# Kernel optimization log

Measured on AMD Instinct MI355X. Metric: run time of the kernel, lower is better.

## Reference

```python
import jax, jax.numpy as jnp
import numpy as np
import math

B, T, D = 2, 2048, 1024
DC, DM, H = 512, 1536, 16
DE, DG = 4096, 1024
EPS = 1e-5
NEG = -1e30


def _layernorm(x, w, b):
    mu = jnp.mean(x, axis=-1, keepdims=True)
    var = jnp.mean(jnp.square(x - mu), axis=-1, keepdims=True)
    return (x - mu) * jax.lax.rsqrt(var + EPS) * w + b


def setup_inputs() -> dict:
    key = jax.random.key(0)
    ks = jax.random.split(key, 12)
    s = 0.02
    x = jax.random.normal(ks[0], (B, T, D), jnp.float32)
    mask = jnp.tril(jnp.ones((T, T), jnp.int32))[None, None]  # [1,1,T,T] causal
    return {
        "x": x,
        "mask": mask,
        "ln1_w": jnp.ones((D,), jnp.float32),
        "ln1_b": jnp.zeros((D,), jnp.float32),
        "wq": jax.random.normal(ks[1], (D, DC), jnp.float32) * s,
        "bq": jnp.zeros((DC,), jnp.float32),
        "wk": jax.random.normal(ks[2], (D, DC), jnp.float32) * s,
        "bk": jnp.zeros((DC,), jnp.float32),
        "wv": jax.random.normal(ks[3], (D, DM), jnp.float32) * s,
        "bv": jnp.zeros((DM,), jnp.float32),
        "wo": jax.random.normal(ks[4], (DM, D), jnp.float32) * s,
        "bo": jnp.zeros((D,), jnp.float32),
        "ln2_w": jnp.ones((D,), jnp.float32),
        "ln2_b": jnp.zeros((D,), jnp.float32),
        "we": jax.random.normal(ks[5], (D, DE), jnp.float32) * s,
        "be": jnp.zeros((DE,), jnp.float32),
        "wg": jax.random.normal(ks[6], (D, DG), jnp.float32) * s,
        "bg": jnp.zeros((DG,), jnp.float32),
        "wu": jax.random.normal(ks[7], (DG, DE), jnp.float32) * s,
        "bu": jnp.zeros((DE,), jnp.float32),
        "wc": jax.random.normal(ks[8], (DE, D), jnp.float32) * s,
        "bc": jnp.zeros((D,), jnp.float32),
    }


def reference(x, mask, ln1_w, ln1_b, wq, bq, wk, bk, wv, bv, wo, bo,
              ln2_w, ln2_b, we, be, wg, bg, wu, bu, wc, bc):
    b, t, _ = x.shape
    chd, mhd = DC // H, DM // H
    # --- attention sublayer ---
    x1 = _layernorm(x, ln1_w, ln1_b)
    q = (x1 @ wq + bq).reshape(b, t, H, chd).transpose(0, 2, 1, 3)  # [b,h,t,chd]
    k = (x1 @ wk + bk).reshape(b, t, H, chd).transpose(0, 2, 1, 3)
    v = (x1 @ wv + bv).reshape(b, t, H, mhd).transpose(0, 2, 1, 3)  # [b,h,t,mhd]
    sc = jnp.einsum('bhqd,bhkd->bhqk', q, k) / math.sqrt(chd)
    sc = jnp.where(mask == 0, NEG, sc)
    attn = jax.nn.softmax(sc, axis=-1)
    y = jnp.einsum('bhqk,bhkd->bhqd', attn, v)  # [b,h,t,mhd]
    y = y.transpose(0, 2, 1, 3).reshape(b, t, DM)
    x = x + (y @ wo + bo)
    # --- FFN sublayer (double-gated SiLU) ---
    x2 = _layernorm(x, ln2_w, ln2_b)
    e = x2 @ we + be
    g = jax.nn.sigmoid(jax.nn.silu(x2 @ wg + bg) @ wu + bu)
    return x + (jax.nn.silu(e * g) @ wc + bc)
```

## Files before the change

### kernel.cpp

```cpp
#include <hip/hip_runtime.h>
#include <hip/hip_bf16.h>

typedef __bf16 bf16x8_t __attribute__((ext_vector_type(8)));
typedef float f32x4_t __attribute__((ext_vector_type(4)));

#define B_ 2
#define T_ 2048
#define D_ 1024
#define DC_ 512
#define DM_ 1536
#define H_ 16
#define DE_ 4096
#define DG_ 1024
#define ROWS (B_*T_)
#define QS_ 2560
#define EG_ 5120
#define MB (1u<<20)

#define GPTR(p) ((const __attribute__((address_space(1))) unsigned int*)(p))
#define LPTR(p) ((__attribute__((address_space(3))) unsigned int*)(p))

__device__ __forceinline__ float sigmoid_f(float x) { return 1.f / (1.f + __expf(-x)); }

__global__ __launch_bounds__(256)
void transpose_cast(const float* __restrict__ W, __hip_bfloat16* __restrict__ Wt,
                    int K, int N) {
    __shared__ float t[32][33];
    const int n0 = blockIdx.x * 32, k0 = blockIdx.y * 32;
    const int tx = threadIdx.x, ty = threadIdx.y;
#pragma unroll
    for (int r = 0; r < 4; ++r)
        t[ty + r * 8][tx] = W[(size_t)(k0 + ty + r * 8) * N + n0 + tx];
    __syncthreads();
#pragma unroll
    for (int r = 0; r < 4; ++r)
        Wt[(size_t)(n0 + ty + r * 8) * K + k0 + tx] = __float2bfloat16(t[tx][ty + r * 8]);
}

__global__ __launch_bounds__(256)
void concat_bias3(const float* __restrict__ a, int na, const float* __restrict__ b,
                  int nb, const float* __restrict__ c, int n, float* __restrict__ o) {
    const int i = blockIdx.x * 256 + threadIdx.x;
    if (i < n)
        o[i] = i < na ? a[i] : (i < na + nb ? b[i - na] : c[i - na - nb]);
}

__global__ __launch_bounds__(256)
void transpose_v(const __hip_bfloat16* __restrict__ QKV, __hip_bfloat16* __restrict__ Vt) {
    __shared__ __hip_bfloat16 t[32][33];
    const int bh = blockIdx.z;
    const int b = bh >> 4, h = bh & 15;
    const int t0 = blockIdx.x * 32;
    const int d0 = blockIdx.y * 32;
    const int tx = threadIdx.x, ty = threadIdx.y;
#pragma unroll
    for (int r = 0; r < 4; ++r)
        t[ty + r * 8][tx] = QKV[(size_t)(b * T_ + t0 + ty + r * 8) * QS_ + 1024 + h * 96 + d0 + tx];
    __syncthreads();
#pragma unroll
    for (int r = 0; r < 4; ++r)
        Vt[((size_t)bh * 96 + d0 + ty + r * 8) * T_ + t0 + tx] = t[tx][ty + r * 8];
}

__global__ __launch_bounds__(256)
void ln_cast(const float* __restrict__ x, const float* __restrict__ w,
             const float* __restrict__ b, __hip_bfloat16* __restrict__ out) {
    const int row = blockIdx.x;
    const int tid = threadIdx.x;
    const float4 v = ((const float4*)(x + (size_t)row * D_))[tid];
    float s = v.x + v.y + v.z + v.w;
#pragma unroll
    for (int o = 32; o; o >>= 1) s += __shfl_down(s, o);
    __shared__ float red1[4], red2[4];
    if (!(tid & 63)) red1[tid >> 6] = s;
    __syncthreads();
    const float mu = (red1[0] + red1[1] + red1[2] + red1[3]) * (1.f / D_);
    const float dx = v.x - mu, dy = v.y - mu, dz = v.z - mu, dw = v.w - mu;
    float s2 = dx * dx + dy * dy + dz * dz + dw * dw;
#pragma unroll
    for (int o = 32; o; o >>= 1) s2 += __shfl_down(s2, o);
    if (!(tid & 63)) red2[tid >> 6] = s2;
    __syncthreads();
    const float var = (red2[0] + red2[1] + red2[2] + red2[3]) * (1.f / D_);
    const float rs = rsqrtf(var + 1e-5f);
    const float4 wv = ((const float4*)w)[tid];
    const float4 bv = ((const float4*)b)[tid];
    __hip_bfloat16* op = out + (size_t)row * D_ + tid * 4;
    op[0] = __float2bfloat16(dx * rs * wv.x + bv.x);
    op[1] = __float2bfloat16(dy * rs * wv.y + bv.y);
    op[2] = __float2bfloat16(dz * rs * wv.z + bv.z);
    op[3] = __float2bfloat16(dw * rs * wv.w + bv.w);
}

template <int EPI, int BM, int BN>
__global__ __launch_bounds__(256)
void gemm_bt(const __hip_bfloat16* __restrict__ A, const __hip_bfloat16* __restrict__ Bt,
             const float* __restrict__ bias, const float* __restrict__ resid,
             const __hip_bfloat16* __restrict__ Ein,
             void* __restrict__ C0, void* __restrict__ C1, int M, int N, int K) {
    constexpr int MI = BM / 32, NJ = BN / 32;
    constexpr size_t STAGE_BYTES = (size_t)(BM + BN) * 128;
    constexpr size_t EPI_BYTES = (EPI == 1) ? (size_t)BM * (BN + 4) * 4
                                            : (size_t)BM * (BN + 8) * 2;
    constexpr size_t SMEM_BYTES = STAGE_BYTES > EPI_BYTES ? STAGE_BYTES : EPI_BYTES;
    __shared__ __align__(16) unsigned char smem[SMEM_BYTES];
    __hip_bfloat16* As0 = (__hip_bfloat16*)smem;
    __hip_bfloat16* Bs0 = As0 + BM * 32;
    __hip_bfloat16* As1 = Bs0 + BN * 32;
    __hip_bfloat16* Bs1 = As1 + BM * 32;

    const int tid = threadIdx.x;
    const int m0 = blockIdx.y * BM;
    const int n0 = blockIdx.x * BN;
    const int lane = tid & 63;
    const int wave = tid >> 6;
    const int wm = (wave >> 1) * (BM / 2), wn = (wave & 1) * (BN / 2);
    const int quad = lane >> 4;
    const int lr = lane & 15;

    auto stage = [&](int k0, __hip_bfloat16* Asd, __hip_bfloat16* Bsd) {
#pragma unroll
        for (int p = 0; p < BM / 64; ++p) {
            const int s = p * 256 + tid;
            const int row = s >> 2;
            const int kc2 = (s & 3) ^ ((row >> 1) & 3);
            __builtin_amdgcn_global_load_lds(
                GPTR(A + (size_t)(m0 + row) * K + k0 + kc2 * 8),
                LPTR(Asd + s * 8), 16, 0, 0);
        }
#pragma unroll
        for (int p = 0; p < BN / 64; ++p) {
            const int s = p * 256 + tid;
            const int row = s >> 2;
            const int kc2 = (s & 3) ^ ((row >> 1) & 3);
            __builtin_amdgcn_global_load_lds(
                GPTR(Bt + (size_t)(n0 + row) * K + k0 + kc2 * 8),
                LPTR(Bsd + s * 8), 16, 0, 0);
        }
    };

    f32x4_t acc[MI][NJ] = {};
    stage(0, As0, Bs0);
    const int kiters = K >> 5;
    for (int k = 0; k < kiters; ++k) {
        __syncthreads();
        const __hip_bfloat16* Ar = (k & 1) ? As1 : As0;
        const __hip_bfloat16* Br = (k & 1) ? Bs1 : Bs0;
        if (k + 1 < kiters)
            stage((k + 1) << 5, (k & 1) ? As0 : As1, (k & 1) ? Bs0 : Bs1);
        bf16x8_t af[MI], bfr[NJ];
#pragma unroll
        for (int i = 0; i < MI; ++i) {
            const int row = wm + i * 16 + lr;
            af[i] = *(const bf16x8_t*)(Ar + (row * 4 + (quad ^ ((row >> 1) & 3))) * 8);
        }
#pragma unroll
        for (int j = 0; j < NJ; ++j) {
            const int row = wn + j * 16 + lr;
            bfr[j] = *(const bf16x8_t*)(Br + (row * 4 + (quad ^ ((row >> 1) & 3))) * 8);
        }
#pragma unroll
        for (int i = 0; i < MI; ++i)
#pragma unroll
            for (int j = 0; j < NJ; ++j)
                acc[i][j] = __builtin_amdgcn_mfma_f32_16x16x32_bf16(af[i], bfr[j], acc[i][j], 0, 0, 0);
    }
    __syncthreads();

    if (EPI == 1) {
        float* Ct = (float*)smem;
        constexpr int LDC = BN + 4;
#pragma unroll
        for (int j = 0; j < NJ; ++j) {
            const float bj = bias[n0 + wn + j * 16 + lr];
#pragma unroll
            for (int i = 0; i < MI; ++i)
#pragma unroll
                for (int r = 0; r < 4; ++r)
                    Ct[(wm + i * 16 + quad * 4 + r) * LDC + wn + j * 16 + lr] =
                        acc[i][j][r] + bj;
        }
        __syncthreads();
        constexpr int CH = BN / 4;
#pragma unroll
        for (int p = 0; p < BM * CH / 256; ++p) {
            const int s = p * 256 + tid;
            const int row = s / CH, ch = s % CH;
            float4 t = *(const float4*)(&Ct[row * LDC + ch * 4]);
            const size_t o = (size_t)(m0 + row) * N + n0 + ch * 4;
            const float4 rv = *(const float4*)(resid + o);
            t.x += rv.x; t.y += rv.y; t.z += rv.z; t.w += rv.w;
            *(float4*)((float*)C0 + o) = t;
        }
    } else {
        __hip_bfloat16* Ct = (__hip_bfloat16*)smem;
        constexpr int LDC = BN + 8;
        const bool gsilu = (EPI == 5) && (n0 >= DE_);
#pragma unroll
        for (int j = 0; j < NJ; ++j) {
            const float bj = bias[n0 + wn + j * 16 + lr];
#pragma unroll
            for (int i = 0; i < MI; ++i)
#pragma unroll
                for (int r = 0; r < 4; ++r) {
                    float v = acc[i][j][r] + bj;
                    if (EPI == 4) v = sigmoid_f(v);
                    else if (EPI == 5) { if (gsilu) v = v * sigmoid_f(v); }
                    Ct[(wm + i * 16 + quad * 4 + r) * LDC + wn + j * 16 + lr] =
                        __float2bfloat16(v);
                }
        }
        __syncthreads();
        constexpr int CH = BN / 8;
#pragma unroll
        for (int p = 0; p < BM * CH / 256; ++p) {
            const int s = p * 256 + tid;
            const int row = s / CH, ch = s % CH;
            union { uint4 u; __hip_bfloat16 h[8]; } tv, ev, ov;
            tv.u = *(const uint4*)(&Ct[row * LDC + ch * 8]);
            if (EPI == 4) {
                const size_t o = (size_t)(m0 + row) * N + n0 + ch * 8;
                ev.u = *(const uint4*)(Ein + o);
#pragma unroll
                for (int q = 0; q < 8; ++q) {
                    const float z = __bfloat162float(ev.h[q]) * __bfloat162float(tv.h[q]);
                    ov.h[q] = __float2bfloat16(z * sigmoid_f(z));
                }
                *(uint4*)((__hip_bfloat16*)C0 + o) = ov.u;
            } else if (EPI == 5) {
                if (n0 < DE_)
                    *(uint4*)((__hip_bfloat16*)C0 + (size_t)(m0 + row) * DE_ + n0 + ch * 8) = tv.u;
                else
                    *(uint4*)((__hip_bfloat16*)C1 + (size_t)(m0 + row) * DG_ + (n0 - DE_) + ch * 8) = tv.u;
            } else {
                *(uint4*)((__hip_bfloat16*)C0 + (size_t)(m0 + row) * N + n0 + ch * 8) = tv.u;
            }
        }
    }
}

__global__ __launch_bounds__(256)
void attn_mfma(const __hip_bfloat16* __restrict__ QKV, const __hip_bfloat16* __restrict__ Vt,
               __hip_bfloat16* __restrict__ Y) {
    __shared__ __hip_bfloat16 Ks[128][40];
    __shared__ __hip_bfloat16 Vts[96][136];
    __shared__ __hip_bfloat16 Ps[4][16][72];
    const int tid = threadIdx.x;
    const int lane = tid & 63;
    const int w = tid >> 6;
    const int c = lane & 15;
    const int quad = lane >> 4;
    const int bh = blockIdx.y;
    const int b = bh >> 4, h = bh & 15;
    const size_t qbase = (size_t)b * T_ * QS_ + h * 32;
    const size_t kbase = qbase + 512;
    const size_t vtbase = (size_t)bh * 96 * T_;
    const size_t ybase = (size_t)b * T_ * DM_ + h * 96;
    const float scale2 = 0.17677669529663687f * 1.4426950408889634f;

    for (int half = 0; half < 2; ++half) {
        const int qt = half ? (31 - (int)blockIdx.x) : (int)blockIdx.x;
        const int q0 = qt * 64;
        const int ntiles = (qt >> 1) + 1;
        const int qrow_a = q0 + w * 16 + c;
        const bf16x8_t qf = *(const bf16x8_t*)(QKV + qbase + (size_t)qrow_a * QS_ + quad * 8);

        f32x4_t o[6] = {};
        float mrow[4], lrow[4];
#pragma unroll
        for (int r = 0; r < 4; ++r) { mrow[r] = -1e30f; lrow[r] = 0.f; }
        const int row_c = q0 + w * 16 + quad * 4;

        for (int t = 0; t < ntiles; ++t) {
            const int k0 = t * 128;
#pragma unroll
            for (int p = 0; p < 2; ++p) {
                const int idx = p * 256 + tid;
                const int kr = idx >> 2, cc = idx & 3;
                *(uint4*)(&Ks[kr][cc * 8]) =
                    *(const uint4*)(QKV + kbase + (size_t)(k0 + kr) * QS_ + cc * 8);
            }
#pragma unroll
            for (int p = 0; p < 6; ++p) {
                const int idx = p * 256 + tid;
                const int vr = idx >> 4, vc = idx & 15;
                *(uint4*)(&Vts[vr][vc * 8]) =
                    *(const uint4*)(Vt + vtbase + (size_t)vr * T_ + k0 + vc * 8);
            }
            __syncthreads();

            f32x4_t s[8];
#pragma unroll
            for (int t2 = 0; t2 < 8; ++t2) {
                const bf16x8_t kf = *(const bf16x8_t*)(&Ks[t2 * 16 + c][quad * 8]);
                f32x4_t z = {0.f, 0.f, 0.f, 0.f};
                s[t2] = __builtin_amdgcn_mfma_f32_16x16x32_bf16(qf, kf, z, 0, 0, 0);
            }

            float p[8][4];
            const bool needmask = (k0 + 128 > q0);
            if (needmask) {
#pragma unroll
                for (int t2 = 0; t2 < 8; ++t2) {
                    const int col = k0 + t2 * 16 + c;
#pragma unroll
                    for (int r = 0; r < 4; ++r) {
                        float v = s[t2][r] * scale2;
                        if (col > row_c + r) v = -1e30f;
                        p[t2][r] = v;
                    }
                }
            } else {
#pragma unroll
                for (int t2 = 0; t2 < 8; ++t2)
#pragma unroll
                    for (int r = 0; r < 4; ++r) p[t2][r] = s[t2][r] * scale2;
            }

#pragma unroll
            for (int r = 0; r < 4; ++r) {
                float mx = p[0][r];
#pragma unroll
                for (int t2 = 1; t2 < 8; ++t2) mx = fmaxf(mx, p[t2][r]);
#pragma unroll
                for (int o2 = 1; o2 < 16; o2 <<= 1) mx = fmaxf(mx, __shfl_xor(mx, o2));
                const float mnew = fmaxf(mrow[r], mx);
                const float alpha = exp2f(mrow[r] - mnew);
                mrow[r] = mnew;
                float rsum = 0.f;
#pragma unroll
                for (int t2 = 0; t2 < 8; ++t2) {
                    p[t2][r] = exp2f(p[t2][r] - mnew);
                    rsum += p[t2][r];
                }
#pragma unroll
                for (int o2 = 1; o2 < 16; o2 <<= 1) rsum += __shfl_xor(rsum, o2);
                lrow[r] = lrow[r] * alpha + rsum;
#pragma unroll
                for (int nb = 0; nb < 6; ++nb) o[nb][r] *= alpha;
            }

#pragma unroll
            for (int hh = 0; hh < 2; ++hh) {
#pragma unroll
                for (int t2 = 0; t2 < 4; ++t2)
#pragma unroll
                    for (int r = 0; r < 4; ++r)
                        Ps[w][quad * 4 + r][t2 * 16 + c] = __float2bfloat16(p[hh * 4 + t2][r]);
                const bf16x8_t pf0 = *(const bf16x8_t*)(&Ps[w][c][quad * 8]);
                const bf16x8_t pf1 = *(const bf16x8_t*)(&Ps[w][c][32 + quad * 8]);
#pragma unroll
                for (int nb = 0; nb < 6; ++nb) {
                    const bf16x8_t vf0 = *(const bf16x8_t*)(&Vts[nb * 16 + c][hh * 64 + quad * 8]);
                    o[nb] = __builtin_amdgcn_mfma_f32_16x16x32_bf16(pf0, vf0, o[nb], 0, 0, 0);
                    const bf16x8_t vf1 = *(const bf16x8_t*)(&Vts[nb * 16 + c][hh * 64 + 32 + quad * 8]);
                    o[nb] = __builtin_amdgcn_mfma_f32_16x16x32_bf16(pf1, vf1, o[nb], 0, 0, 0);
                }
            }
            __syncthreads();
        }

#pragma unroll
        for (int r = 0; r < 4; ++r) {
            const float inv = 1.f / lrow[r];
            const size_t rowoff = ybase + (size_t)(row_c + r) * DM_;
#pragma unroll
            for (int nb = 0; nb < 6; ++nb)
                Y[rowoff + nb * 16 + c] = __float2bfloat16(o[nb][r] * inv);
        }
    }
}

extern "C" void kernel_launch(void* const* d_in, const int* in_sizes, int n_in,
                              void* d_out, int out_size, void* d_ws, size_t ws_size,
                              hipStream_t stream) {
    const float* x     = (const float*)d_in[0];
    const float* ln1_w = (const float*)d_in[2];
    const float* ln1_b = (const float*)d_in[3];
    const float* wq = (const float*)d_in[4];  const float* bq = (const float*)d_in[5];
    const float* wk = (const float*)d_in[6];  const float* bk = (const float*)d_in[7];
    const float* wv = (const float*)d_in[8];  const float* bv = (const float*)d_in[9];
    const float* wo = (const float*)d_in[10]; const float* bo = (const float*)d_in[11];
    const float* ln2_w = (const float*)d_in[12];
    const float* ln2_b = (const float*)d_in[13];
    const float* we = (const float*)d_in[14]; const float* be = (const float*)d_in[15];
    const float* wg = (const float*)d_in[16]; const float* bg = (const float*)d_in[17];
    const float* wu = (const float*)d_in[18]; const float* bu = (const float*)d_in[19];
    const float* wc = (const float*)d_in[20]; const float* bc = (const float*)d_in[21];
    float* out = (float*)d_out;

    char* ws = (char*)d_ws;
    typedef __hip_bfloat16 bf16;
    bf16* wqkvT = (bf16*)(ws + (size_t) 0 * MB);
    bf16* wqT   = wqkvT;
    bf16* wkT   = (bf16*)(ws + (size_t) 1 * MB);
    bf16* wvT   = (bf16*)(ws + (size_t) 2 * MB);
    bf16* woT   = (bf16*)(ws + (size_t) 5 * MB);
    bf16* wewgT = (bf16*)(ws + (size_t) 8 * MB);
    bf16* weT   = wewgT;
    bf16* wgT   = (bf16*)(ws + (size_t)16 * MB);
    bf16* wuT   = (bf16*)(ws + (size_t)18 * MB);
    bf16* wcT   = (bf16*)(ws + (size_t)26 * MB);
    float* bqkv = (float*)(ws + (size_t)34 * MB);
    float* bewg = (float*)(ws + (size_t)34 * MB + 65536);
    bf16* x1b   = (bf16*)(ws + (size_t)35 * MB);
    bf16* x2b   = x1b;
    bf16* qkv   = (bf16*)(ws + (size_t)43 * MB);
    float* xmid = (float*)(ws + (size_t)43 * MB);
    bf16* vt    = (bf16*)(ws + (size_t)63 * MB);
    bf16* yb    = (bf16*)(ws + (size_t)75 * MB);
    bf16* eb    = (bf16*)(ws + (size_t)59 * MB);
    bf16* hb    = (bf16*)(ws + (size_t)91 * MB);

    const dim3 tb(32, 8);
    transpose_cast<<<dim3(DC_ / 32, D_ / 32), tb, 0, stream>>>(wq, wqT, D_, DC_);
    transpose_cast<<<dim3(DC_ / 32, D_ / 32), tb, 0, stream>>>(wk, wkT, D_, DC_);
    transpose_cast<<<dim3(DM_ / 32, D_ / 32), tb, 0, stream>>>(wv, wvT, D_, DM_);
    transpose_cast<<<dim3(D_ / 32, DM_ / 32), tb, 0, stream>>>(wo, woT, DM_, D_);
    transpose_cast<<<dim3(DE_ / 32, D_ / 32), tb, 0, stream>>>(we, weT, D_, DE_);
    transpose_cast<<<dim3(DG_ / 32, D_ / 32), tb, 0, stream>>>(wg, wgT, D_, DG_);
    transpose_cast<<<dim3(DE_ / 32, DG_ / 32), tb, 0, stream>>>(wu, wuT, DG_, DE_);
    transpose_cast<<<dim3(D_ / 32, DE_ / 32), tb, 0, stream>>>(wc, wcT, DE_, D_);
    concat_bias3<<<(QS_ + 255) / 256, 256, 0, stream>>>(bq, 512, bk, 512, bv, QS_, bqkv);
    concat_bias3<<<(EG_ + 255) / 256, 256, 0, stream>>>(be, DE_, bg, DG_, nullptr, EG_, bewg);

    ln_cast<<<ROWS, 256, 0, stream>>>(x, ln1_w, ln1_b, x1b);

    gemm_bt<0, 128, 128><<<dim3(QS_ / 128, ROWS / 128), 256, 0, stream>>>(
        x1b, wqkvT, bqkv, nullptr, nullptr, qkv, nullptr, ROWS, QS_, D_);

    transpose_v<<<dim3(T_ / 32, 3, B_ * H_), tb, 0, stream>>>(qkv, vt);

    attn_mfma<<<dim3(16, B_ * H_), 256, 0, stream>>>(qkv, vt, yb);

    gemm_bt<1, 64, 64><<<dim3(D_ / 64, ROWS / 64), 256, 0, stream>>>(
        yb, woT, bo, x, nullptr, xmid, nullptr, ROWS, D_, DM_);

    ln_cast<<<ROWS, 256, 0, stream>>>(xmid, ln2_w, ln2_b, x2b);

    gemm_bt<5, 128, 128><<<dim3(EG_ / 128, ROWS / 128), 256, 0, stream>>>(
        x2b, wewgT, bewg, nullptr, nullptr, eb, hb, ROWS, EG_, D_);

    gemm_bt<4, 128, 128><<<dim3(DE_ / 128, ROWS / 128), 256, 0, stream>>>(
        hb, wuT, bu, nullptr, eb, eb, nullptr, ROWS, DE_, DG_);

    gemm_bt<1, 64, 64><<<dim3(D_ / 64, ROWS / 64), 256, 0, stream>>>(
        eb, wcT, bc, xmid, nullptr, out, nullptr, ROWS, D_, DE_);
}
```

Measured before the change: 517.6 us.

## Batch weight transposes into one launch and restructure attention kernel layout

The eight per-weight transpose launches become a single kernel that looks up its source, destination and shape in a table, removing per-launch overhead. The attention kernel is reworked: K and V^T tiles are loaded straight into swizzled LDS with global_load_lds, and the QK MFMA operands are swapped so each lane owns one query row. That ownership shrinks the softmax reductions to two shuffles and lets P feed the PV MFMA from registers with zero-padded half-K operands instead of round-tripping through LDS. Block indices are also remapped to group heads for locality. The padded PV MFMAs do twice the MFMA issue for the same useful work.

```diff
diff --git a/kernel.cpp b/kernel.cpp
--- a/kernel.cpp
+++ b/kernel.cpp
@@ -22,11 +22,26 @@
 
 __device__ __forceinline__ float sigmoid_f(float x) { return 1.f / (1.f + __expf(-x)); }
 
-__global__ __launch_bounds__(256)
-void transpose_cast(const float* __restrict__ W, __hip_bfloat16* __restrict__ Wt,
-                    int K, int N) {
+struct TCTab {
+    const float* src[8];
+    __hip_bfloat16* dst[8];
+    int K[8], N[8];
+    int off[8];
+};
+
+__global__ __launch_bounds__(256)
+void transpose_cast_all(TCTab tab) {
     __shared__ float t[32][33];
-    const int n0 = blockIdx.x * 32, k0 = blockIdx.y * 32;
+    const int bid = blockIdx.x;
+    int sidx = 0;
+#pragma unroll
+    for (int i = 1; i < 8; ++i) sidx = (bid >= tab.off[i]) ? i : sidx;
+    const float* __restrict__ W = tab.src[sidx];
+    __hip_bfloat16* __restrict__ Wt = tab.dst[sidx];
+    const int K = tab.K[sidx], N = tab.N[sidx];
+    const int local = bid - tab.off[sidx];
+    const int nx = N >> 5;
+    const int n0 = (local % nx) * 32, k0 = (local / nx) * 32;
     const int tx = threadIdx.x, ty = threadIdx.y;
 #pragma unroll
     for (int r = 0; r < 4; ++r)
@@ -242,15 +257,17 @@
 __global__ __launch_bounds__(256)
 void attn_mfma(const __hip_bfloat16* __restrict__ QKV, const __hip_bfloat16* __restrict__ Vt,
                __hip_bfloat16* __restrict__ Y) {
-    __shared__ __hip_bfloat16 Ks[128][40];
-    __shared__ __hip_bfloat16 Vts[96][136];
-    __shared__ __hip_bfloat16 Ps[4][16][72];
+    __shared__ __align__(16) __hip_bfloat16 Ks[128 * 32];
+    __shared__ __align__(16) __hip_bfloat16 VTS[96 * 128];
     const int tid = threadIdx.x;
     const int lane = tid & 63;
     const int w = tid >> 6;
     const int c = lane & 15;
     const int quad = lane >> 4;
-    const int bh = blockIdx.y;
+    const int nlin = blockIdx.y * 16 + blockIdx.x;
+    const int x8 = nlin & 7, mm = nlin >> 3;
+    const int bh = x8 * 4 + (mm >> 4);
+    const int qpair = mm & 15;
     const int b = bh >> 4, h = bh & 15;
     const size_t qbase = (size_t)b * T_ * QS_ + h * 32;
     const size_t kbase = qbase + 512;
@@ -259,54 +276,56 @@
     const float scale2 = 0.17677669529663687f * 1.4426950408889634f;
 
     for (int half = 0; half < 2; ++half) {
-        const int qt = half ? (31 - (int)blockIdx.x) : (int)blockIdx.x;
+        const int qt = half ? (31 - qpair) : qpair;
         const int q0 = qt * 64;
         const int ntiles = (qt >> 1) + 1;
-        const int qrow_a = q0 + w * 16 + c;
-        const bf16x8_t qf = *(const bf16x8_t*)(QKV + qbase + (size_t)qrow_a * QS_ + quad * 8);
+        const int qrow = q0 + w * 16 + c;
+        const bf16x8_t qf = *(const bf16x8_t*)(QKV + qbase + (size_t)qrow * QS_ + quad * 8);
 
         f32x4_t o[6] = {};
-        float mrow[4], lrow[4];
-#pragma unroll
-        for (int r = 0; r < 4; ++r) { mrow[r] = -1e30f; lrow[r] = 0.f; }
-        const int row_c = q0 + w * 16 + quad * 4;
+        float mrow = -1e30f, lrow = 0.f;
 
         for (int t = 0; t < ntiles; ++t) {
             const int k0 = t * 128;
 #pragma unroll
             for (int p = 0; p < 2; ++p) {
-                const int idx = p * 256 + tid;
-                const int kr = idx >> 2, cc = idx & 3;
-                *(uint4*)(&Ks[kr][cc * 8]) =
-                    *(const uint4*)(QKV + kbase + (size_t)(k0 + kr) * QS_ + cc * 8);
+                const int s = p * 256 + tid;
+                const int row = s >> 2;
+                const int ch = (s & 3) ^ ((row >> 1) & 3);
+                __builtin_amdgcn_global_load_lds(
+                    GPTR(QKV + kbase + (size_t)(k0 + row) * QS_ + ch * 8),
+                    LPTR(Ks + s * 8), 16, 0, 0);
             }
 #pragma unroll
             for (int p = 0; p < 6; ++p) {
-                const int idx = p * 256 + tid;
-                const int vr = idx >> 4, vc = idx & 15;
-                *(uint4*)(&Vts[vr][vc * 8]) =
-                    *(const uint4*)(Vt + vtbase + (size_t)vr * T_ + k0 + vc * 8);
+                const int s = p * 256 + tid;
+                const int vr = s >> 4;
+                const int ch = (s & 15) ^ (vr & 15);
+                __builtin_amdgcn_global_load_lds(
+                    GPTR(Vt + vtbase + (size_t)vr * T_ + k0 + ch * 8),
+                    LPTR(VTS + s * 8), 16, 0, 0);
             }
             __syncthreads();
 
             f32x4_t s[8];
 #pragma unroll
             for (int t2 = 0; t2 < 8; ++t2) {
-                const bf16x8_t kf = *(const bf16x8_t*)(&Ks[t2 * 16 + c][quad * 8]);
+                const int krow = t2 * 16 + c;
+                const bf16x8_t kf =
+                    *(const bf16x8_t*)(Ks + (krow * 4 + (quad ^ ((krow >> 1) & 3))) * 8);
                 f32x4_t z = {0.f, 0.f, 0.f, 0.f};
-                s[t2] = __builtin_amdgcn_mfma_f32_16x16x32_bf16(qf, kf, z, 0, 0, 0);
+                s[t2] = __builtin_amdgcn_mfma_f32_16x16x32_bf16(kf, qf, z, 0, 0, 0);
             }
 
             float p[8][4];
-            const bool needmask = (k0 + 128 > q0);
-            if (needmask) {
+            if (k0 + 128 > q0) {
 #pragma unroll
                 for (int t2 = 0; t2 < 8; ++t2) {
-                    const int col = k0 + t2 * 16 + c;
+                    const int kk = k0 + t2 * 16 + quad * 4;
 #pragma unroll
                     for (int r = 0; r < 4; ++r) {
                         float v = s[t2][r] * scale2;
-                        if (col > row_c + r) v = -1e30f;
+                        if (kk + r > qrow) v = -1e30f;
                         p[t2][r] = v;
                     }
                 }
@@ -317,56 +336,65 @@
                     for (int r = 0; r < 4; ++r) p[t2][r] = s[t2][r] * scale2;
             }
 
-#pragma unroll
-            for (int r = 0; r < 4; ++r) {
-                float mx = p[0][r];
-#pragma unroll
-                for (int t2 = 1; t2 < 8; ++t2) mx = fmaxf(mx, p[t2][r]);
-#pragma unroll
-                for (int o2 = 1; o2 < 16; o2 <<= 1) mx = fmaxf(mx, __shfl_xor(mx, o2));
-                const float mnew = fmaxf(mrow[r], mx);
-                const float alpha = exp2f(mrow[r] - mnew);
-                mrow[r] = mnew;
-                float rsum = 0.f;
-#pragma unroll
-                for (int t2 = 0; t2 < 8; ++t2) {
+            float mx = p[0][0];
+#pragma unroll
+            for (int t2 = 0; t2 < 8; ++t2)
+#pragma unroll
+                for (int r = 0; r < 4; ++r) mx = fmaxf(mx, p[t2][r]);
+            mx = fmaxf(mx, __shfl_xor(mx, 16));
+            mx = fmaxf(mx, __shfl_xor(mx, 32));
+            const float mnew = fmaxf(mrow, mx);
+            const float alpha = exp2f(mrow - mnew);
+            mrow = mnew;
+            float rsum = 0.f;
+#pragma unroll
+            for (int t2 = 0; t2 < 8; ++t2)
+#pragma unroll
+                for (int r = 0; r < 4; ++r) {
                     p[t2][r] = exp2f(p[t2][r] - mnew);
                     rsum += p[t2][r];
                 }
-#pragma unroll
-                for (int o2 = 1; o2 < 16; o2 <<= 1) rsum += __shfl_xor(rsum, o2);
-                lrow[r] = lrow[r] * alpha + rsum;
-#pragma unroll
-                for (int nb = 0; nb < 6; ++nb) o[nb][r] *= alpha;
-            }
-
-#pragma unroll
-            for (int hh = 0; hh < 2; ++hh) {
-#pragma unroll
-                for (int t2 = 0; t2 < 4; ++t2)
-#pragma unroll
-                    for (int r = 0; r < 4; ++r)
-                        Ps[w][quad * 4 + r][t2 * 16 + c] = __float2bfloat16(p[hh * 4 + t2][r]);
-                const bf16x8_t pf0 = *(const bf16x8_t*)(&Ps[w][c][quad * 8]);
-                const bf16x8_t pf1 = *(const bf16x8_t*)(&Ps[w][c][32 + quad * 8]);
+            rsum += __shfl_xor(rsum, 16);
+            rsum += __shfl_xor(rsum, 32);
+            lrow = lrow * alpha + rsum;
+
+            float arow[4];
+#pragma unroll
+            for (int r = 0; r < 4; ++r) arow[r] = __shfl(alpha, quad * 20 + r);
+#pragma unroll
+            for (int nb = 0; nb < 6; ++nb)
+#pragma unroll
+                for (int r = 0; r < 4; ++r) o[nb][r] *= arow[r];
+
+#pragma unroll
+            for (int t2 = 0; t2 < 8; ++t2) {
+                union { bf16x8_t v; __hip_bfloat16 h[8]; unsigned int u[4]; } au;
+                au.u[2] = 0; au.u[3] = 0;
+#pragma unroll
+                for (int r = 0; r < 4; ++r) au.h[r] = __float2bfloat16(p[t2][r]);
 #pragma unroll
                 for (int nb = 0; nb < 6; ++nb) {
-                    const bf16x8_t vf0 = *(const bf16x8_t*)(&Vts[nb * 16 + c][hh * 64 + quad * 8]);
-                    o[nb] = __builtin_amdgcn_mfma_f32_16x16x32_bf16(pf0, vf0, o[nb], 0, 0, 0);
-                    const bf16x8_t vf1 = *(const bf16x8_t*)(&Vts[nb * 16 + c][hh * 64 + 32 + quad * 8]);
-                    o[nb] = __builtin_amdgcn_mfma_f32_16x16x32_bf16(pf1, vf1, o[nb], 0, 0, 0);
+                    const int vr = nb * 16 + c;
+                    const int slot = (2 * t2 + (quad >> 1)) ^ (vr & 15);
+                    union { bf16x8_t v; unsigned int u[4]; } bu;
+                    const uint2 vv = *(const uint2*)(VTS + (vr * 16 + slot) * 8 + (quad & 1) * 4);
+                    bu.u[0] = vv.x; bu.u[1] = vv.y; bu.u[2] = 0; bu.u[3] = 0;
+                    o[nb] = __builtin_amdgcn_mfma_f32_16x16x32_bf16(au.v, bu.v, o[nb], 0, 0, 0);
                 }
             }
             __syncthreads();
         }
 
+        const float linv = 1.f / lrow;
+        float lr4[4];
+#pragma unroll
+        for (int r = 0; r < 4; ++r) lr4[r] = __shfl(linv, quad * 20 + r);
 #pragma unroll
         for (int r = 0; r < 4; ++r) {
-            const float inv = 1.f / lrow[r];
-            const size_t rowoff = ybase + (size_t)(row_c + r) * DM_;
+            const size_t rowoff = ybase + (size_t)(q0 + w * 16 + quad * 4 + r) * DM_;
 #pragma unroll
             for (int nb = 0; nb < 6; ++nb)
-                Y[rowoff + nb * 16 + c] = __float2bfloat16(o[nb][r] * inv);
+                Y[rowoff + nb * 16 + c] = __float2bfloat16(o[nb][r] * lr4[r]);
         }
     }
 }
@@ -412,15 +440,16 @@
     bf16* eb    = (bf16*)(ws + (size_t)59 * MB);
     bf16* hb    = (bf16*)(ws + (size_t)91 * MB);
 
-    const dim3 tb(32, 8);
-    transpose_cast<<<dim3(DC_ / 32, D_ / 32), tb, 0, stream>>>(wq, wqT, D_, DC_);
-    transpose_cast<<<dim3(DC_ / 32, D_ / 32), tb, 0, stream>>>(wk, wkT, D_, DC_);
-    transpose_cast<<<dim3(DM_ / 32, D_ / 32), tb, 0, stream>>>(wv, wvT, D_, DM_);
-    transpose_cast<<<dim3(D_ / 32, DM_ / 32), tb, 0, stream>>>(wo, woT, DM_, D_);
-    transpose_cast<<<dim3(DE_ / 32, D_ / 32), tb, 0, stream>>>(we, weT, D_, DE_);
-    transpose_cast<<<dim3(DG_ / 32, D_ / 32), tb, 0, stream>>>(wg, wgT, D_, DG_);
-    transpose_cast<<<dim3(DE_ / 32, DG_ / 32), tb, 0, stream>>>(wu, wuT, DG_, DE_);
-    transpose_cast<<<dim3(D_ / 32, DE_ / 32), tb, 0, stream>>>(wc, wcT, DE_, D_);
+    TCTab tab;
+    tab.src[0] = wq; tab.dst[0] = wqT; tab.K[0] = D_;  tab.N[0] = DC_; tab.off[0] = 0;
+    tab.src[1] = wk; tab.dst[1] = wkT; tab.K[1] = D_;  tab.N[1] = DC_; tab.off[1] = 512;
+    tab.src[2] = wv; tab.dst[2] = wvT; tab.K[2] = D_;  tab.N[2] = DM_; tab.off[2] = 1024;
+    tab.src[3] = wo; tab.dst[3] = woT; tab.K[3] = DM_; tab.N[3] = D_;  tab.off[3] = 2560;
+    tab.src[4] = we; tab.dst[4] = weT; tab.K[4] = D_;  tab.N[4] = DE_; tab.off[4] = 4096;
+    tab.src[5] = wg; tab.dst[5] = wgT; tab.K[5] = D_;  tab.N[5] = DG_; tab.off[5] = 8192;
+    tab.src[6] = wu; tab.dst[6] = wuT; tab.K[6] = DG_; tab.N[6] = DE_; tab.off[6] = 9216;
+    tab.src[7] = wc; tab.dst[7] = wcT; tab.K[7] = DE_; tab.N[7] = D_;  tab.off[7] = 13312;
+    transpose_cast_all<<<17408, dim3(32, 8), 0, stream>>>(tab);
     concat_bias3<<<(QS_ + 255) / 256, 256, 0, stream>>>(bq, 512, bk, 512, bv, QS_, bqkv);
     concat_bias3<<<(EG_ + 255) / 256, 256, 0, stream>>>(be, DE_, bg, DG_, nullptr, EG_, bewg);
 
@@ -429,7 +458,7 @@
     gemm_bt<0, 128, 128><<<dim3(QS_ / 128, ROWS / 128), 256, 0, stream>>>(
         x1b, wqkvT, bqkv, nullptr, nullptr, qkv, nullptr, ROWS, QS_, D_);
 
-    transpose_v<<<dim3(T_ / 32, 3, B_ * H_), tb, 0, stream>>>(qkv, vt);
+    transpose_v<<<dim3(T_ / 32, 3, B_ * H_), dim3(32, 8), 0, stream>>>(qkv, vt);
 
     attn_mfma<<<dim3(16, B_ * H_), 256, 0, stream>>>(qkv, vt, yb);
 
```

After: 493.0 us. 1.05x faster.
